# Kernel tuning notes

Hardware: AMD Instinct MI355X
Metric: run time of the kernel (lower is better)

## Reference

```python
import jax, jax.numpy as jnp
import numpy as np

EMBED_DIM = 2048
NUM_HEADS = 32
NUM_KV_HEADS = 8
HEAD_DIM = EMBED_DIM // NUM_HEADS          # 64
GROUP = NUM_HEADS // NUM_KV_HEADS          # 4 queries per KV head
BATCH, SEQ = 2, 2048


def setup_inputs() -> dict:
    key = jax.random.key(0)
    ks = jax.random.split(key, 9)
    s_in = 1.0 / np.sqrt(EMBED_DIM)
    kv_dim = NUM_KV_HEADS * HEAD_DIM
    return {
        "x":      jax.random.normal(ks[0], (BATCH, SEQ, EMBED_DIM), jnp.float32),
        "Wq":     jax.random.normal(ks[1], (EMBED_DIM, EMBED_DIM), jnp.float32) * s_in,
        "bq":     jnp.zeros((EMBED_DIM,), jnp.float32),
        "Wk":     jax.random.normal(ks[2], (EMBED_DIM, kv_dim), jnp.float32) * s_in,
        "bk":     jnp.zeros((kv_dim,), jnp.float32),
        "Wv":     jax.random.normal(ks[3], (EMBED_DIM, kv_dim), jnp.float32) * s_in,
        "bv":     jnp.zeros((kv_dim,), jnp.float32),
        "Wo":     jax.random.normal(ks[4], (EMBED_DIM, EMBED_DIM), jnp.float32) * s_in,
        "bo":     jnp.zeros((EMBED_DIM,), jnp.float32),
    }


def reference(x, Wq, bq, Wk, bk, Wv, bv, Wo, bo):
    B, S, _ = x.shape
    # Projections (torch Linear == x @ W + b with W stored as [in, out] here)
    q = (x @ Wq + bq).reshape(B, S, NUM_KV_HEADS, GROUP, HEAD_DIM)  # grouped heads
    k = (x @ Wk + bk).reshape(B, S, NUM_KV_HEADS, HEAD_DIM)
    v = (x @ Wv + bv).reshape(B, S, NUM_KV_HEADS, HEAD_DIM)

    scale = 1.0 / np.sqrt(HEAD_DIM)
    # scores[b, h, g, s, t] = q[b, s, h, g, :] . k[b, t, h, :]
    # (repeat_interleave of K across the group dim == broadcasting over g)
    scores = jnp.einsum("bshgd,bthd->bhgst", q, k) * scale
    attn = jax.nn.softmax(scores, axis=-1)
    out = jnp.einsum("bhgst,bthd->bshgd", attn, v)  # [B, S, kvh, g, D]
    out = out.reshape(B, S, EMBED_DIM)
    return out @ Wo + bo
```

## Files before the change

kernel.cpp:

```cpp
#include <hip/hip_runtime.h>


typedef __attribute__((ext_vector_type(8)))  short bf16x8;
typedef __attribute__((ext_vector_type(4)))  float f32x4;
typedef __attribute__((ext_vector_type(16))) float f32x16;

#define DEVI static __device__ __forceinline__

#if __has_builtin(__builtin_amdgcn_exp2f)
#define EXP2F __builtin_amdgcn_exp2f
#else
#define EXP2F exp2f
#endif

DEVI short f2b(float f){
  unsigned u = __builtin_bit_cast(unsigned, f);
  u += 0x7FFFu + ((u >> 16) & 1u);
  return (short)(u >> 16);
}
DEVI unsigned pack2(float a, float b){
  unsigned ua = __builtin_bit_cast(unsigned, a) + 0x8000u;
  unsigned ub = __builtin_bit_cast(unsigned, b) + 0x8000u;
  return __builtin_amdgcn_perm(ub, ua, 0x07060302u);
}

typedef __attribute__((address_space(3))) unsigned       lds_u32;
typedef __attribute__((address_space(1))) const unsigned gbl_u32;
DEVI void glds16(const short* g, short* l){
  __builtin_amdgcn_global_load_lds((gbl_u32*)g, (lds_u32*)l, 16, 0, 0);
}

__global__ void cast_kernel(const float* __restrict__ in, short* __restrict__ out, int n){
  int i = (blockIdx.x * 256 + threadIdx.x) * 8;
  if(i >= n) return;
  float4 a = *(const float4*)(in + i);
  float4 b = *(const float4*)(in + i + 4);
  bf16x8 v;
  v[0]=f2b(a.x); v[1]=f2b(a.y); v[2]=f2b(a.z); v[3]=f2b(a.w);
  v[4]=f2b(b.x); v[5]=f2b(b.y); v[6]=f2b(b.z); v[7]=f2b(b.w);
  *(bf16x8*)(out + i) = v;
}

__global__ void prep_kernel(const float* __restrict__ Wq, const float* __restrict__ Wk,
                            const float* __restrict__ Wv, const float* __restrict__ Wo,
                            const float* __restrict__ bq, const float* __restrict__ bk,
                            const float* __restrict__ bv,
                            short* __restrict__ WT, short* __restrict__ WoT,
                            float* __restrict__ bqkv){
  __shared__ __align__(16) short tile[64*72];
  const int gy = blockIdx.y;
  const int t = threadIdx.x;
  if(gy >= 80){
    int i = blockIdx.x * 256 + t;
    if(i < 3072) bqkv[i] = (i < 2048) ? bq[i] : (i < 2560 ? bk[i-2048] : bv[i-2560]);
    return;
  }
  const float* src; short* dst; int ldin, by;
  if(gy < 32)      { src = Wq; dst = WT;             ldin = 2048; by = gy;    }
  else if(gy < 40) { src = Wk; dst = WT + 2048*2048; ldin =  512; by = gy-32; }
  else if(gy < 48) { src = Wv; dst = WT + 2560*2048; ldin =  512; by = gy-40; }
  else             { src = Wo; dst = WoT;            ldin = 2048; by = gy-48; }
  const int tr = blockIdx.x * 64;
  const int tc = by * 64;
  for(int c = t; c < 512; c += 256){
    int r = c >> 3, g = c & 7;
    const float* p = src + (size_t)(tr + r) * ldin + tc + g*8;
    bf16x8 v;
    #pragma unroll
    for(int e = 0; e < 8; e++) v[e] = f2b(p[e]);
    *(bf16x8*)&tile[r*72 + g*8] = v;
  }
  __syncthreads();
  for(int c = t; c < 512; c += 256){
    int r = c >> 3, g = c & 7;
    bf16x8 v;
    #pragma unroll
    for(int e = 0; e < 8; e++) v[e] = tile[(g*8+e)*72 + r];
    *(bf16x8*)(dst + (size_t)(tc + r) * 2048 + tr + g*8) = v;
  }
}

__global__ void transpose_bf16_kernel(const short* __restrict__ in, short* __restrict__ out,
                                      int ldin, int ldout){
  __shared__ __align__(16) short tile[64*72];
  const int tr = blockIdx.x * 64;
  const int tc = blockIdx.y * 64;
  const int t = threadIdx.x;
  for(int c = t; c < 512; c += 256){
    int r = c >> 3, g = c & 7;
    *(bf16x8*)&tile[r*72 + g*8] = *(const bf16x8*)(in + (size_t)(tr + r) * ldin + tc + g*8);
  }
  __syncthreads();
  for(int c = t; c < 512; c += 256){
    int r = c >> 3, g = c & 7;
    bf16x8 v;
    #pragma unroll
    for(int e = 0; e < 8; e++) v[e] = tile[(g*8+e)*72 + r];
    *(bf16x8*)(out + (size_t)(tc + r) * ldout + tr + g*8) = v;
  }
}

template<bool OUT_F32>
__global__ __launch_bounds__(256, 2)
void gemm_bt_kernel(const short* __restrict__ A, const short* __restrict__ BT,
                    const float* __restrict__ bias, void* __restrict__ C,
                    int M, int N, int K, int scale_cols, float qscale){
  __shared__ __align__(16) short As[128*32];
  __shared__ __align__(16) short Bs[128*32];
  const int m0 = blockIdx.x * 128;
  const int n0 = blockIdx.y * 128;
  const int tid = threadIdx.x;
  const int wave = tid >> 6, lane = tid & 63;
  const int l16 = lane & 15, quad = lane >> 4;
  const int wm = (wave >> 1) * 64, wn = (wave & 1) * 64;

  const short* gA = A  + (size_t)(m0 + wave*32 + (lane>>2))*K + (lane&3)*8;
  const short* gB = BT + (size_t)(n0 + wave*32 + (lane>>2))*K + (lane&3)*8;
  short* lA = As + wave*32*32;
  short* lB = Bs + wave*32*32;

  f32x4 acc[4][4];
  #pragma unroll
  for(int i=0;i<4;i++)
    #pragma unroll
    for(int j=0;j<4;j++) acc[i][j] = (f32x4)(0.0f);

  for(int k0 = 0; k0 < K; k0 += 32){
    glds16(gA + k0,                lA);
    glds16(gA + 16*(size_t)K + k0, lA + 512);
    glds16(gB + k0,                lB);
    glds16(gB + 16*(size_t)K + k0, lB + 512);
    __syncthreads();
    bf16x8 af[4], bfr[4];
    #pragma unroll
    for(int i=0;i<4;i++){
      af[i]  = *(const bf16x8*)&As[(wm + i*16 + l16)*32 + quad*8];
      bfr[i] = *(const bf16x8*)&Bs[(wn + i*16 + l16)*32 + quad*8];
    }
    #pragma unroll
    for(int i=0;i<4;i++)
      #pragma unroll
      for(int j=0;j<4;j++)
        acc[i][j] = __builtin_amdgcn_mfma_f32_16x16x32_bf16(af[i], bfr[j], acc[i][j], 0, 0, 0);
    __syncthreads();
  }

  #pragma unroll
  for(int j=0;j<4;j++){
    int col = n0 + wn + j*16 + l16;
    float bb = bias[col];
    float sc = (col < scale_cols) ? qscale : 1.0f;
    #pragma unroll
    for(int i=0;i<4;i++){
      #pragma unroll
      for(int r=0;r<4;r++){
        size_t row = (size_t)(m0 + wm + i*16 + quad*4 + r);
        float v = (acc[i][j][r] + bb) * sc;
        if(OUT_F32) ((float*)C)[row*(size_t)N + col] = v;
        else        ((short*)C)[row*(size_t)N + col] = f2b(v);
      }
    }
  }
}

__global__ __launch_bounds__(256, 2)
void attn_kernel(const short* __restrict__ Qg, const short* __restrict__ Kg,
                 const short* __restrict__ VT, short* __restrict__ Og, int ldq){
  const int qt  = blockIdx.x;
  const int kvh = blockIdx.y;
  const int b   = blockIdx.z;
  const int tid = threadIdx.x;
  const int wave = tid >> 6, lane = tid & 63;
  const int c = lane & 31, h = lane >> 5;
  const int head = kvh*4 + wave;
  const int q0 = qt * 64;

  __shared__ __align__(16) short Ks[64*72];
  __shared__ __align__(16) short Vs[64*72];
  __shared__ __align__(16) short Ps[4][64*72];
  __shared__ __align__(16) float lS[4][2][32];

  bf16x8 qreg[4][2];
  #pragma unroll
  for(int ks=0; ks<4; ks++)
    #pragma unroll
    for(int qg=0; qg<2; qg++)
      qreg[ks][qg] = *(const bf16x8*)(Qg + (size_t)(b*2048 + q0 + qg*32 + c)*ldq
                                         + head*64 + ks*16 + h*8);

  float lsum[2] = {0.0f, 0.0f};
  f32x16 oacc[2][2];
  #pragma unroll
  for(int qg=0; qg<2; qg++)
    #pragma unroll
    for(int nb=0; nb<2; nb++) oacc[qg][nb] = (f32x16)(0.0f);

  const short* gK = Kg + (size_t)(b*2048 + (tid>>3))*ldq + kvh*64 + (tid&7)*8;
  const short* gV = VT + (size_t)(kvh*64 + (tid>>3))*4096 + b*2048 + (tid&7)*8;
  short* sK = &Ks[(tid>>3)*72 + (tid&7)*8];
  short* sV = &Vs[(tid>>3)*72 + (tid&7)*8];
  const size_t kHalf = (size_t)32 * ldq;

  bf16x8 kr0 = *(const bf16x8*)(gK);
  bf16x8 kr1 = *(const bf16x8*)(gK + kHalf);
  bf16x8 vr0 = *(const bf16x8*)(gV);
  bf16x8 vr1 = *(const bf16x8*)(gV + 32*4096);

  for(int t0 = 0; t0 < 2048; t0 += 64){
    if(t0) __syncthreads();
    *(bf16x8*)sK            = kr0;
    *(bf16x8*)(sK + 32*72)  = kr1;
    *(bf16x8*)sV            = vr0;
    *(bf16x8*)(sV + 32*72)  = vr1;
    __syncthreads();
    if(t0 + 64 < 2048){
      const short* nK = gK + (size_t)(t0 + 64)*ldq;
      const short* nV = gV + (t0 + 64);
      kr0 = *(const bf16x8*)(nK);
      kr1 = *(const bf16x8*)(nK + kHalf);
      vr0 = *(const bf16x8*)(nV);
      vr1 = *(const bf16x8*)(nV + 32*4096);
    }

    f32x16 st[2][2];
    st[0][0] = (f32x16)(0.0f); st[0][1] = (f32x16)(0.0f);
    st[1][0] = (f32x16)(0.0f); st[1][1] = (f32x16)(0.0f);
    #pragma unroll
    for(int ks=0; ks<4; ks++){
      #pragma unroll
      for(int kb=0; kb<2; kb++){
        bf16x8 ak = *(const bf16x8*)&Ks[(kb*32 + c)*72 + ks*16 + h*8];
        st[kb][0] = __builtin_amdgcn_mfma_f32_32x32x16_bf16(ak, qreg[ks][0], st[kb][0], 0, 0, 0);
        st[kb][1] = __builtin_amdgcn_mfma_f32_32x32x16_bf16(ak, qreg[ks][1], st[kb][1], 0, 0, 0);
      }
    }

    #pragma unroll
    for(int qg=0; qg<2; qg++){
      float sum = 0.0f;
      #pragma unroll
      for(int kb=0; kb<2; kb++){
        #pragma unroll
        for(int g2=0; g2<4; g2++){
          float p0 = EXP2F(st[kb][qg][g2*4+0]);
          float p1 = EXP2F(st[kb][qg][g2*4+1]);
          float p2 = EXP2F(st[kb][qg][g2*4+2]);
          float p3 = EXP2F(st[kb][qg][g2*4+3]);
          sum += (p0 + p1) + (p2 + p3);
          uint2 w; w.x = pack2(p0, p1); w.y = pack2(p2, p3);
          *(uint2*)&Ps[wave][(qg*32 + c)*72 + kb*32 + g2*8 + 4*h] = w;
        }
      }
      lsum[qg] += sum;
    }

    #pragma unroll
    for(int ks=0; ks<4; ks++){
      bf16x8 ap0 = *(const bf16x8*)&Ps[wave][(c     )*72 + ks*16 + h*8];
      bf16x8 ap1 = *(const bf16x8*)&Ps[wave][(32 + c)*72 + ks*16 + h*8];
      #pragma unroll
      for(int nb=0; nb<2; nb++){
        bf16x8 av = *(const bf16x8*)&Vs[(nb*32 + c)*72 + ks*16 + h*8];
        oacc[0][nb] = __builtin_amdgcn_mfma_f32_32x32x16_bf16(ap0, av, oacc[0][nb], 0, 0, 0);
        oacc[1][nb] = __builtin_amdgcn_mfma_f32_32x32x16_bf16(ap1, av, oacc[1][nb], 0, 0, 0);
      }
    }
  }

  #pragma unroll
  for(int qg=0; qg<2; qg++){
    lsum[qg] += __shfl_xor(lsum[qg], 32);
    if(h == 0) lS[wave][qg][c] = lsum[qg];
  }
  __builtin_amdgcn_s_waitcnt(0);
  #pragma unroll
  for(int qg=0; qg<2; qg++){
    f32x4 l4[4];
    #pragma unroll
    for(int g2=0; g2<4; g2++){
      f32x4 t = *(const f32x4*)&lS[wave][qg][8*g2 + 4*h];
      l4[g2][0]=1.0f/t[0]; l4[g2][1]=1.0f/t[1]; l4[g2][2]=1.0f/t[2]; l4[g2][3]=1.0f/t[3];
    }
    #pragma unroll
    for(int nb=0; nb<2; nb++){
      int col = head*64 + nb*32 + c;
      #pragma unroll
      for(int e=0; e<16; e++){
        int row = q0 + qg*32 + (e&3) + 8*(e>>2) + 4*h;
        Og[(size_t)(b*2048 + row)*2048 + col] = f2b(oacc[qg][e>>4==0?nb:nb][e] * l4[e>>2][e&3]);
      }
    }
  }
}

extern "C" void kernel_launch(void* const* d_in, const int* in_sizes, int n_in,
                              void* d_out, int out_size, void* d_ws, size_t ws_size,
                              hipStream_t stream){
  const float* x  = (const float*)d_in[0];
  const float* Wq = (const float*)d_in[1];
  const float* bq = (const float*)d_in[2];
  const float* Wk = (const float*)d_in[3];
  const float* bk = (const float*)d_in[4];
  const float* Wv = (const float*)d_in[5];
  const float* bv = (const float*)d_in[6];
  const float* Wo = (const float*)d_in[7];
  const float* bo = (const float*)d_in[8];

  char* ws = (char*)d_ws;
  short* WT   = (short*)(ws);
  short* WoT  = (short*)(ws + 25165824);
  short* xb   = (short*)(ws + 33554432);
  short* QKV  = (short*)(ws + 50331648);
  short* VTb  = (short*)(ws + 75497472);
  float* bqkv = (float*)(ws + 79691776);
  short* AO   = xb;

  cast_kernel<<<4096, 256, 0, stream>>>(x, xb, 8388608);
  prep_kernel<<<dim3(32,81), 256, 0, stream>>>(Wq, Wk, Wv, Wo, bq, bk, bv, WT, WoT, bqkv);

  gemm_bt_kernel<false><<<dim3(32,24), 256, 0, stream>>>(xb, WT, bqkv, QKV,
                                                         4096, 3072, 2048,
                                                         2048, 0.1803368801111244f);

  transpose_bf16_kernel<<<dim3(64,8), 256, 0, stream>>>(QKV + 2560, VTb, 3072, 4096);

  attn_kernel<<<dim3(32,8,2), 256, 0, stream>>>(QKV, QKV + 2048, VTb, AO, 3072);

  gemm_bt_kernel<true><<<dim3(32,16), 256, 0, stream>>>(AO, WoT, bo, (float*)d_out,
                                                        4096, 2048, 2048, 0, 1.0f);
}
```

Measured before the change: 312.6 us.

## Switch to fp16 MFMA and keep softmax probabilities in registers for PV

Converts all intermediates from bf16 to fp16 and uses the f16 MFMA variants. The attention kernel is restructured so that P is computed per 32-key block and fed directly from registers into the PV MFMA, with V as the A operand in a transposed formulation. This removes the per-wave P staging round trip through LDS and the lS scratch buffer. K/V tiles are double-buffered in LDS, which drops one barrier per iteration, and the epilogue writes packed outputs directly. fp16 trades exponent range for mantissa precision, so unnormalized exp2 scores and the GEMM intermediates could overflow if the values are large.

```diff
diff --git a/kernel.cpp b/kernel.cpp
--- a/kernel.cpp
+++ b/kernel.cpp
@@ -1,9 +1,11 @@
 #include <hip/hip_runtime.h>
 
 
-typedef __attribute__((ext_vector_type(8)))  short bf16x8;
-typedef __attribute__((ext_vector_type(4)))  float f32x4;
-typedef __attribute__((ext_vector_type(16))) float f32x16;
+typedef __attribute__((ext_vector_type(8)))  short     s16x8;
+typedef __attribute__((ext_vector_type(8)))  _Float16  h8;
+typedef __attribute__((ext_vector_type(2)))  __fp16    fp16x2;
+typedef __attribute__((ext_vector_type(4)))  float     f32x4;
+typedef __attribute__((ext_vector_type(16))) float     f32x16;
 
 #define DEVI static __device__ __forceinline__
 
@@ -13,15 +15,10 @@
 #define EXP2F exp2f
 #endif
 
-DEVI short f2b(float f){
-  unsigned u = __builtin_bit_cast(unsigned, f);
-  u += 0x7FFFu + ((u >> 16) & 1u);
-  return (short)(u >> 16);
-}
-DEVI unsigned pack2(float a, float b){
-  unsigned ua = __builtin_bit_cast(unsigned, a) + 0x8000u;
-  unsigned ub = __builtin_bit_cast(unsigned, b) + 0x8000u;
-  return __builtin_amdgcn_perm(ub, ua, 0x07060302u);
+DEVI short f2h(float f){ _Float16 h = (_Float16)f; return __builtin_bit_cast(short, h); }
+DEVI unsigned pkh(float a, float b){
+  fp16x2 t = __builtin_amdgcn_cvt_pkrtz(a, b);
+  return __builtin_bit_cast(unsigned, t);
 }
 
 typedef __attribute__((address_space(3))) unsigned       lds_u32;
@@ -35,10 +32,10 @@
   if(i >= n) return;
   float4 a = *(const float4*)(in + i);
   float4 b = *(const float4*)(in + i + 4);
-  bf16x8 v;
-  v[0]=f2b(a.x); v[1]=f2b(a.y); v[2]=f2b(a.z); v[3]=f2b(a.w);
-  v[4]=f2b(b.x); v[5]=f2b(b.y); v[6]=f2b(b.z); v[7]=f2b(b.w);
-  *(bf16x8*)(out + i) = v;
+  s16x8 v;
+  v[0]=f2h(a.x); v[1]=f2h(a.y); v[2]=f2h(a.z); v[3]=f2h(a.w);
+  v[4]=f2h(b.x); v[5]=f2h(b.y); v[6]=f2h(b.z); v[7]=f2h(b.w);
+  *(s16x8*)(out + i) = v;
 }
 
 __global__ void prep_kernel(const float* __restrict__ Wq, const float* __restrict__ Wk,
@@ -65,38 +62,38 @@
   for(int c = t; c < 512; c += 256){
     int r = c >> 3, g = c & 7;
     const float* p = src + (size_t)(tr + r) * ldin + tc + g*8;
-    bf16x8 v;
-    #pragma unroll
-    for(int e = 0; e < 8; e++) v[e] = f2b(p[e]);
-    *(bf16x8*)&tile[r*72 + g*8] = v;
+    s16x8 v;
+    #pragma unroll
+    for(int e = 0; e < 8; e++) v[e] = f2h(p[e]);
+    *(s16x8*)&tile[r*72 + g*8] = v;
   }
   __syncthreads();
   for(int c = t; c < 512; c += 256){
     int r = c >> 3, g = c & 7;
-    bf16x8 v;
+    s16x8 v;
     #pragma unroll
     for(int e = 0; e < 8; e++) v[e] = tile[(g*8+e)*72 + r];
-    *(bf16x8*)(dst + (size_t)(tc + r) * 2048 + tr + g*8) = v;
-  }
-}
-
-__global__ void transpose_bf16_kernel(const short* __restrict__ in, short* __restrict__ out,
-                                      int ldin, int ldout){
+    *(s16x8*)(dst + (size_t)(tc + r) * 2048 + tr + g*8) = v;
+  }
+}
+
+__global__ void transpose_h_kernel(const short* __restrict__ in, short* __restrict__ out,
+                                   int ldin, int ldout){
   __shared__ __align__(16) short tile[64*72];
   const int tr = blockIdx.x * 64;
   const int tc = blockIdx.y * 64;
   const int t = threadIdx.x;
   for(int c = t; c < 512; c += 256){
     int r = c >> 3, g = c & 7;
-    *(bf16x8*)&tile[r*72 + g*8] = *(const bf16x8*)(in + (size_t)(tr + r) * ldin + tc + g*8);
+    *(s16x8*)&tile[r*72 + g*8] = *(const s16x8*)(in + (size_t)(tr + r) * ldin + tc + g*8);
   }
   __syncthreads();
   for(int c = t; c < 512; c += 256){
     int r = c >> 3, g = c & 7;
-    bf16x8 v;
+    s16x8 v;
     #pragma unroll
     for(int e = 0; e < 8; e++) v[e] = tile[(g*8+e)*72 + r];
-    *(bf16x8*)(out + (size_t)(tc + r) * ldout + tr + g*8) = v;
+    *(s16x8*)(out + (size_t)(tc + r) * ldout + tr + g*8) = v;
   }
 }
 
@@ -131,17 +128,17 @@
     glds16(gB + k0,                lB);
     glds16(gB + 16*(size_t)K + k0, lB + 512);
     __syncthreads();
-    bf16x8 af[4], bfr[4];
+    h8 af[4], bfr[4];
     #pragma unroll
     for(int i=0;i<4;i++){
-      af[i]  = *(const bf16x8*)&As[(wm + i*16 + l16)*32 + quad*8];
-      bfr[i] = *(const bf16x8*)&Bs[(wn + i*16 + l16)*32 + quad*8];
+      af[i]  = *(const h8*)&As[(wm + i*16 + l16)*32 + quad*8];
+      bfr[i] = *(const h8*)&Bs[(wn + i*16 + l16)*32 + quad*8];
     }
     #pragma unroll
     for(int i=0;i<4;i++)
       #pragma unroll
       for(int j=0;j<4;j++)
-        acc[i][j] = __builtin_amdgcn_mfma_f32_16x16x32_bf16(af[i], bfr[j], acc[i][j], 0, 0, 0);
+        acc[i][j] = __builtin_amdgcn_mfma_f32_16x16x32_f16(af[i], bfr[j], acc[i][j], 0, 0, 0);
     __syncthreads();
   }
 
@@ -157,7 +154,7 @@
         size_t row = (size_t)(m0 + wm + i*16 + quad*4 + r);
         float v = (acc[i][j][r] + bb) * sc;
         if(OUT_F32) ((float*)C)[row*(size_t)N + col] = v;
-        else        ((short*)C)[row*(size_t)N + col] = f2b(v);
+        else        ((short*)C)[row*(size_t)N + col] = f2h(v);
       }
     }
   }
@@ -175,94 +172,98 @@
   const int head = kvh*4 + wave;
   const int q0 = qt * 64;
 
-  __shared__ __align__(16) short Ks[64*72];
-  __shared__ __align__(16) short Vs[64*72];
-  __shared__ __align__(16) short Ps[4][64*72];
-  __shared__ __align__(16) float lS[4][2][32];
-
-  bf16x8 qreg[4][2];
-  #pragma unroll
-  for(int ks=0; ks<4; ks++)
+  __shared__ __align__(16) short Ks[2][64*72];
+  __shared__ __align__(16) short Vs[2][64*72];
+
+  h8 qreg[4][2];
+  #pragma unroll
+  for(int ks2=0; ks2<4; ks2++)
     #pragma unroll
     for(int qg=0; qg<2; qg++)
-      qreg[ks][qg] = *(const bf16x8*)(Qg + (size_t)(b*2048 + q0 + qg*32 + c)*ldq
-                                         + head*64 + ks*16 + h*8);
+      qreg[ks2][qg] = *(const h8*)(Qg + (size_t)(b*2048 + q0 + qg*32 + c)*ldq
+                                      + head*64 + ks2*16 + h*8);
 
   float lsum[2] = {0.0f, 0.0f};
   f32x16 oacc[2][2];
   #pragma unroll
   for(int qg=0; qg<2; qg++)
     #pragma unroll
-    for(int nb=0; nb<2; nb++) oacc[qg][nb] = (f32x16)(0.0f);
+    for(int mb=0; mb<2; mb++) oacc[qg][mb] = (f32x16)(0.0f);
 
   const short* gK = Kg + (size_t)(b*2048 + (tid>>3))*ldq + kvh*64 + (tid&7)*8;
   const short* gV = VT + (size_t)(kvh*64 + (tid>>3))*4096 + b*2048 + (tid&7)*8;
-  short* sK = &Ks[(tid>>3)*72 + (tid&7)*8];
-  short* sV = &Vs[(tid>>3)*72 + (tid&7)*8];
+  const int so = (tid>>3)*72 + (tid&7)*8;
   const size_t kHalf = (size_t)32 * ldq;
 
-  bf16x8 kr0 = *(const bf16x8*)(gK);
-  bf16x8 kr1 = *(const bf16x8*)(gK + kHalf);
-  bf16x8 vr0 = *(const bf16x8*)(gV);
-  bf16x8 vr1 = *(const bf16x8*)(gV + 32*4096);
+  s16x8 kr0 = *(const s16x8*)(gK);
+  s16x8 kr1 = *(const s16x8*)(gK + kHalf);
+  s16x8 vr0 = *(const s16x8*)(gV);
+  s16x8 vr1 = *(const s16x8*)(gV + 32*4096);
 
   for(int t0 = 0; t0 < 2048; t0 += 64){
-    if(t0) __syncthreads();
-    *(bf16x8*)sK            = kr0;
-    *(bf16x8*)(sK + 32*72)  = kr1;
-    *(bf16x8*)sV            = vr0;
-    *(bf16x8*)(sV + 32*72)  = vr1;
+    const int buf = (t0 >> 6) & 1;
+    short* sK = &Ks[buf][so];
+    short* sV = &Vs[buf][so];
+    *(s16x8*)sK           = kr0;
+    *(s16x8*)(sK + 32*72) = kr1;
+    *(s16x8*)sV           = vr0;
+    *(s16x8*)(sV + 32*72) = vr1;
     __syncthreads();
     if(t0 + 64 < 2048){
       const short* nK = gK + (size_t)(t0 + 64)*ldq;
       const short* nV = gV + (t0 + 64);
-      kr0 = *(const bf16x8*)(nK);
-      kr1 = *(const bf16x8*)(nK + kHalf);
-      vr0 = *(const bf16x8*)(nV);
-      vr1 = *(const bf16x8*)(nV + 32*4096);
-    }
-
-    f32x16 st[2][2];
-    st[0][0] = (f32x16)(0.0f); st[0][1] = (f32x16)(0.0f);
-    st[1][0] = (f32x16)(0.0f); st[1][1] = (f32x16)(0.0f);
-    #pragma unroll
-    for(int ks=0; ks<4; ks++){
-      #pragma unroll
-      for(int kb=0; kb<2; kb++){
-        bf16x8 ak = *(const bf16x8*)&Ks[(kb*32 + c)*72 + ks*16 + h*8];
-        st[kb][0] = __builtin_amdgcn_mfma_f32_32x32x16_bf16(ak, qreg[ks][0], st[kb][0], 0, 0, 0);
-        st[kb][1] = __builtin_amdgcn_mfma_f32_32x32x16_bf16(ak, qreg[ks][1], st[kb][1], 0, 0, 0);
-      }
-    }
-
-    #pragma unroll
-    for(int qg=0; qg<2; qg++){
-      float sum = 0.0f;
-      #pragma unroll
-      for(int kb=0; kb<2; kb++){
+      kr0 = *(const s16x8*)(nK);
+      kr1 = *(const s16x8*)(nK + kHalf);
+      vr0 = *(const s16x8*)(nV);
+      vr1 = *(const s16x8*)(nV + 32*4096);
+    }
+    const short* Kbuf = Ks[buf];
+    const short* Vbuf = Vs[buf];
+
+    #pragma unroll
+    for(int kb=0; kb<2; kb++){
+      f32x16 st[2];
+      st[0] = (f32x16)(0.0f); st[1] = (f32x16)(0.0f);
+      #pragma unroll
+      for(int ks2=0; ks2<4; ks2++){
+        h8 ak = *(const h8*)&Kbuf[(kb*32 + c)*72 + ks2*16 + h*8];
+        st[0] = __builtin_amdgcn_mfma_f32_32x32x16_f16(ak, qreg[ks2][0], st[0], 0, 0, 0);
+        st[1] = __builtin_amdgcn_mfma_f32_32x32x16_f16(ak, qreg[ks2][1], st[1], 0, 0, 0);
+      }
+
+      union H8U { h8 v; unsigned u[4]; };
+      H8U pk[2][2];
+      #pragma unroll
+      for(int qg=0; qg<2; qg++){
+        float sacc = 0.0f;
         #pragma unroll
-        for(int g2=0; g2<4; g2++){
-          float p0 = EXP2F(st[kb][qg][g2*4+0]);
-          float p1 = EXP2F(st[kb][qg][g2*4+1]);
-          float p2 = EXP2F(st[kb][qg][g2*4+2]);
-          float p3 = EXP2F(st[kb][qg][g2*4+3]);
-          sum += (p0 + p1) + (p2 + p3);
-          uint2 w; w.x = pack2(p0, p1); w.y = pack2(p2, p3);
-          *(uint2*)&Ps[wave][(qg*32 + c)*72 + kb*32 + g2*8 + 4*h] = w;
+        for(int j=0; j<4; j++){
+          float pa = EXP2F(st[qg][2*j]);
+          float pb = EXP2F(st[qg][2*j+1]);
+          sacc += pa + pb;
+          pk[qg][0].u[j] = pkh(pa, pb);
         }
-      }
-      lsum[qg] += sum;
-    }
-
-    #pragma unroll
-    for(int ks=0; ks<4; ks++){
-      bf16x8 ap0 = *(const bf16x8*)&Ps[wave][(c     )*72 + ks*16 + h*8];
-      bf16x8 ap1 = *(const bf16x8*)&Ps[wave][(32 + c)*72 + ks*16 + h*8];
-      #pragma unroll
-      for(int nb=0; nb<2; nb++){
-        bf16x8 av = *(const bf16x8*)&Vs[(nb*32 + c)*72 + ks*16 + h*8];
-        oacc[0][nb] = __builtin_amdgcn_mfma_f32_32x32x16_bf16(ap0, av, oacc[0][nb], 0, 0, 0);
-        oacc[1][nb] = __builtin_amdgcn_mfma_f32_32x32x16_bf16(ap1, av, oacc[1][nb], 0, 0, 0);
+        #pragma unroll
+        for(int j=0; j<4; j++){
+          float pa = EXP2F(st[qg][8+2*j]);
+          float pb = EXP2F(st[qg][8+2*j+1]);
+          sacc += pa + pb;
+          pk[qg][1].u[j] = pkh(pa, pb);
+        }
+        lsum[qg] += sacc;
+      }
+
+      #pragma unroll
+      for(int ksp=0; ksp<2; ksp++){
+        #pragma unroll
+        for(int mb=0; mb<2; mb++){
+          const short* vb = &Vbuf[(mb*32 + c)*72 + kb*32 + ksp*16 + h*4];
+          H8U av;
+          *(uint2*)&av.u[0] = *(const uint2*)(vb);
+          *(uint2*)&av.u[2] = *(const uint2*)(vb + 8);
+          oacc[0][mb] = __builtin_amdgcn_mfma_f32_32x32x16_f16(av.v, pk[0][ksp].v, oacc[0][mb], 0, 0, 0);
+          oacc[1][mb] = __builtin_amdgcn_mfma_f32_32x32x16_f16(av.v, pk[1][ksp].v, oacc[1][mb], 0, 0, 0);
+        }
       }
     }
   }
@@ -270,24 +271,17 @@
   #pragma unroll
   for(int qg=0; qg<2; qg++){
     lsum[qg] += __shfl_xor(lsum[qg], 32);
-    if(h == 0) lS[wave][qg][c] = lsum[qg];
-  }
-  __builtin_amdgcn_s_waitcnt(0);
-  #pragma unroll
-  for(int qg=0; qg<2; qg++){
-    f32x4 l4[4];
-    #pragma unroll
-    for(int g2=0; g2<4; g2++){
-      f32x4 t = *(const f32x4*)&lS[wave][qg][8*g2 + 4*h];
-      l4[g2][0]=1.0f/t[0]; l4[g2][1]=1.0f/t[1]; l4[g2][2]=1.0f/t[2]; l4[g2][3]=1.0f/t[3];
-    }
-    #pragma unroll
-    for(int nb=0; nb<2; nb++){
-      int col = head*64 + nb*32 + c;
-      #pragma unroll
-      for(int e=0; e<16; e++){
-        int row = q0 + qg*32 + (e&3) + 8*(e>>2) + 4*h;
-        Og[(size_t)(b*2048 + row)*2048 + col] = f2b(oacc[qg][e>>4==0?nb:nb][e] * l4[e>>2][e&3]);
+    float li = 1.0f / lsum[qg];
+    size_t rowoff = (size_t)(b*2048 + q0 + qg*32 + c)*2048 + head*64;
+    #pragma unroll
+    for(int mb=0; mb<2; mb++){
+      #pragma unroll
+      for(int g2=0; g2<4; g2++){
+        int d0 = mb*32 + 8*g2 + 4*h;
+        uint2 w;
+        w.x = pkh(oacc[qg][mb][4*g2+0]*li, oacc[qg][mb][4*g2+1]*li);
+        w.y = pkh(oacc[qg][mb][4*g2+2]*li, oacc[qg][mb][4*g2+3]*li);
+        *(uint2*)&Og[rowoff + d0] = w;
       }
     }
   }
@@ -322,7 +316,7 @@
                                                          4096, 3072, 2048,
                                                          2048, 0.1803368801111244f);
 
-  transpose_bf16_kernel<<<dim3(64,8), 256, 0, stream>>>(QKV + 2560, VTb, 3072, 4096);
+  transpose_h_kernel<<<dim3(64,8), 256, 0, stream>>>(QKV + 2560, VTb, 3072, 4096);
 
   attn_kernel<<<dim3(32,8,2), 256, 0, stream>>>(QKV, QKV + 2048, VTb, AO, 3072);
 
```

Result: faster. 303.0 us (-3.1%).
